# Optimization experiments

Hardware: AMD Instinct MI355X
Metric: run time of the kernel (lower is better)

The kernel has to match this reference:

```python
import jax, jax.numpy as jnp
import numpy as np

# Winograd F(2x2, 3x3) transform matrices (standard Lavin & Gray form).
# The original torch module encodes B^T / A^T but applies them with elementwise
# mul (a bug that crashes); the intended math is Y = A^T [ (G g G^T) .* (B^T d B) ] A
# per 4x4 input tile with stride 2, which equals a valid 3x3 conv. We implement
# that intended Winograd computation faithfully and vectorized.
_BT = jnp.array([[1., 0., -1., 0.],
                 [0., 1., 1., 0.],
                 [0., -1., 1., 0.],
                 [0., 1., 0., -1.]], dtype=jnp.float32)
_G = jnp.array([[1., 0., 0.],
                [0.5, 0.5, 0.5],
                [0.5, -0.5, 0.5],
                [0., 0., 1.]], dtype=jnp.float32)
_AT = jnp.array([[1., 1., 1., 0.],
                 [0., 1., -1., -1.]], dtype=jnp.float32)


def setup_inputs() -> dict:
    key = jax.random.key(0)
    k1, k2 = jax.random.split(key)
    X = jax.random.normal(k1, (16, 32, 258, 258), dtype=jnp.float32)
    K = jax.random.normal(k2, (32, 32, 3, 3), dtype=jnp.float32)
    return {"X": X, "K": K}


def _winograd_conv(X, K):
    B_, C, H, W = X.shape
    Fo = K.shape[0]
    blocks = (H - 3) // 2 + 1  # number of 2x2 output tiles per spatial dim

    # Kernel transform: U = G K G^T  -> (Fo, C, 4, 4)
    U = jnp.einsum('ij,fcjk,lk->fcil', _G, K, _G)

    # Extract overlapping 4x4 tiles with stride 2: (B, C, blocks, blocks, 4, 4)
    i0 = jnp.arange(blocks) * 2
    win = i0[:, None] + jnp.arange(4)[None, :]          # (blocks, 4)
    tiles = X[:, :, win, :]                              # (B, C, blocks, 4, W)
    tiles = tiles[:, :, :, :, win]                       # (B, C, blocks, 4, blocks, 4)
    tiles = tiles.transpose(0, 1, 2, 4, 3, 5)            # (B, C, p, q, 4, 4)

    # Input transform: V = B^T d B
    V = jnp.einsum('ij,bcpqjk,lk->bcpqil', _BT, tiles, _BT)

    # Elementwise multiply in transform domain, summed over input channels
    M = jnp.einsum('fcil,bcpqil->bfpqil', U, V)          # (B, Fo, p, q, 4, 4)

    # Inverse transform: Y = A^T M A -> (B, Fo, p, q, 2, 2)
    Y = jnp.einsum('ij,bfpqjk,lk->bfpqil', _AT, M, _AT)

    # Stitch 2x2 tiles back: (B, Fo, 2*blocks, 2*blocks)
    out = Y.transpose(0, 1, 2, 4, 3, 5).reshape(B_, Fo, 2 * blocks, 2 * blocks)
    return out


def reference(X, K):
    return _winograd_conv(X, K)
```

## Files before the change

### kernel.cpp

```cpp
#include <hip/hip_runtime.h>
#include <stdint.h>

typedef __attribute__((ext_vector_type(8))) short bf16x8;
typedef __attribute__((ext_vector_type(4))) float f32x4;
typedef __attribute__((ext_vector_type(2))) float f32x2;

__device__ inline float bflo(uint32_t w) { union { uint32_t i; float f; } v; v.i = w << 16; return v.f; }
__device__ inline float bfhi(uint32_t w) { union { uint32_t i; float f; } v; v.i = w & 0xffff0000u; return v.f; }
__device__ inline uint32_t f2bf(float f) { union { float f; uint32_t i; } v; v.f = f; return (v.i + 0x8000u) >> 16; }
__device__ inline uint32_t pk(float lo, float hi) { return f2bf(lo) | (f2bf(hi) << 16); }

__device__ inline f32x2 pka(f32x2 a, f32x2 b) {
    f32x2 d; asm("v_pk_add_f32 %0, %1, %2" : "=v"(d) : "v"(a), "v"(b)); return d;
}
__device__ inline f32x2 pks(f32x2 a, f32x2 b) {
    f32x2 d; asm("v_pk_add_f32 %0, %1, %2 neg_lo:[0,1] neg_hi:[0,1]" : "=v"(d) : "v"(a), "v"(b)); return d;
}
__device__ inline uint32_t cvtpk2(float lo, float hi) {
    uint32_t r; asm("v_cvt_pk_bf16_f32 %0, %1, %2" : "=v"(r) : "v"(lo), "v"(hi)); return r;
}
__device__ inline uint32_t cvtpk(f32x2 v) { return cvtpk2(v.x, v.y); }
__device__ inline f32x2 unpk(uint32_t w) {
    union { uint32_t u; float f; } lo, hi; lo.u = w << 16; hi.u = w & 0xffff0000u;
    return (f32x2){lo.f, hi.f};
}

__global__ __launch_bounds__(256) void wg_filter(const float* __restrict__ Kk, uint32_t* __restrict__ Ud)
{
    const int idx = blockIdx.x * 256 + threadIdx.x;
    if (idx >= 512) return;
    const int cp = idx & 15, f = idx >> 4;
    float u[2][16];
    #pragma unroll
    for (int h = 0; h < 2; h++) {
        const float* kp = Kk + (f * 32 + cp * 2 + h) * 9;
        float k00 = kp[0], k01 = kp[1], k02 = kp[2];
        float k10 = kp[3], k11 = kp[4], k12 = kp[5];
        float k20 = kp[6], k21 = kp[7], k22 = kp[8];
        float t[4][3];
        t[0][0] = k00; t[0][1] = k01; t[0][2] = k02;
        t[1][0] = 0.5f * (k00 + k10 + k20); t[1][1] = 0.5f * (k01 + k11 + k21); t[1][2] = 0.5f * (k02 + k12 + k22);
        t[2][0] = 0.5f * (k00 - k10 + k20); t[2][1] = 0.5f * (k01 - k11 + k21); t[2][2] = 0.5f * (k02 - k12 + k22);
        t[3][0] = k20; t[3][1] = k21; t[3][2] = k22;
        #pragma unroll
        for (int i = 0; i < 4; i++) {
            float a0 = t[i][0], a1 = t[i][1], a2 = t[i][2];
            u[h][i * 4 + 0] = a0;
            u[h][i * 4 + 1] = 0.5f * (a0 + a1 + a2);
            u[h][i * 4 + 2] = 0.5f * (a0 - a1 + a2);
            u[h][i * 4 + 3] = a2;
        }
    }
    const int base = ((cp >> 2) * 32 + f) * 4 + (cp & 3);
    #pragma unroll
    for (int p = 0; p < 16; p++) Ud[p * 512 + base] = pk(u[0][p], u[1][p]);
}

__global__ __launch_bounds__(256, 3) void wg_main(
    const float* __restrict__ X, const uint16_t* __restrict__ U, float* __restrict__ out)
{
    __shared__ __align__(16) uint32_t Pl[2912];
    __shared__ __align__(16) uint16_t Vl[2][4096];

    const int tid = threadIdx.x;
    const int lin  = blockIdx.x + 16 * (blockIdx.y + 32 * blockIdx.z);
    const int work = (lin & 7) * 1024 + (lin >> 3);
    const int qb = work & 15;
    const int pb = (work >> 4) & 31;
    const int b  = work >> 9;
    const int y0 = pb * 8, x0 = qb * 16;

    const int wave = tid >> 6, lane = tid & 63;
    const int fh = wave & 1, tb = wave >> 1;
    const int l15 = lane & 15, lq = lane >> 4;
    const uint16_t* Ub = U + (lq * 32 + fh * 16 + l15) * 8;

    bf16x8 a_cur[4];
    #pragma unroll
    for (int l = 0; l < 4; l++)
        a_cur[l] = *(const bf16x8*)(Ub + l * 1024);

    for (int s = tid; s < 1440; s += 256) {
        const int pr = s / 90;
        const int r  = s - pr * 90;
        const int row = r / 9, seg = r - row * 9;
        const float* g0 = X + ((size_t)((b * 32 + pr * 2) * 258 + y0 + row)) * 258 + x0 + seg * 2;
        float2 a = *(const float2*)g0;
        float2 c = *(const float2*)(g0 + 258 * 258);
        uint2 w;
        w.x = cvtpk2(a.x, c.x);
        w.y = cvtpk2(a.y, c.y);
        *(uint2*)&Pl[pr * 182 + row * 18 + seg * 2] = w;
    }
    __syncthreads();

    const int cp2 = tid & 3, t15c = (tid >> 2) & 15;

    float y[4][4];
    #pragma unroll
    for (int r = 0; r < 4; r++)
        #pragma unroll
        for (int j = 0; j < 4; j++) y[r][j] = 0.f;

    #pragma unroll
    for (int i = 0; i < 4; i++) {
        const int ra = (i == 0) ? 0 : (i == 2) ? 2 : 1;
        const int rb = (i == 3) ? 3 : (i == 2) ? 1 : 2;

        uint32_t* vp = (uint32_t*)Vl[i & 1];

        #pragma unroll
        for (int it = 0; it < 2; it++) {
            const int rem  = it * 4 + wave;
            const int tblk = rem & 1, cpH = rem >> 1;
            const int cp   = cpH * 4 + cp2;
            const int tt   = tblk * 16 + t15c;
            const int tr   = tt >> 3, tc = tt & 7;
            const uint32_t* pp = &Pl[cp * 182 + (tr * 2) * 18 + tc * 2];
            uint2 wa0 = *(const uint2*)&pp[ra * 18];
            uint2 wa1 = *(const uint2*)&pp[ra * 18 + 2];
            uint2 wb0 = *(const uint2*)&pp[rb * 18];
            uint2 wb1 = *(const uint2*)&pp[rb * 18 + 2];
            f32x2 da[4], db[4];
            da[0] = unpk(wa0.x); da[1] = unpk(wa0.y); da[2] = unpk(wa1.x); da[3] = unpk(wa1.y);
            db[0] = unpk(wb0.x); db[1] = unpk(wb0.y); db[2] = unpk(wb1.x); db[3] = unpk(wb1.y);
            f32x2 e[4];
            #pragma unroll
            for (int k = 0; k < 4; k++)
                e[k] = (i == 1) ? pka(da[k], db[k]) : pks(da[k], db[k]);
            const int vbase = ((tblk * 4 + cpH) * 16 + t15c) * 4 + cp2;
            vp[0 * 512 + vbase] = cvtpk(pks(e[0], e[2]));
            vp[1 * 512 + vbase] = cvtpk(pka(e[1], e[2]));
            vp[2 * 512 + vbase] = cvtpk(pks(e[2], e[1]));
            vp[3 * 512 + vbase] = cvtpk(pks(e[1], e[3]));
        }

        bf16x8 a_nxt[4];
        if (i < 3) {
            #pragma unroll
            for (int l = 0; l < 4; l++)
                a_nxt[l] = *(const bf16x8*)(Ub + ((i + 1) * 4 + l) * 1024);
        }

        __syncthreads();

        const uint16_t* Vb = Vl[i & 1] + ((tb * 4 + lq) * 16 + l15) * 8;
        f32x4 acc[4];
        #pragma unroll
        for (int l = 0; l < 4; l++) {
            bf16x8 v = *(const bf16x8*)(Vb + l * 1024);
            acc[l] = __builtin_amdgcn_mfma_f32_16x16x32_bf16(a_cur[l], v,
                        (f32x4){0.f, 0.f, 0.f, 0.f}, 0, 0, 0);
        }

        #pragma unroll
        for (int l = 0; l < 4; l++) a_cur[l] = a_nxt[l];

        #pragma unroll
        for (int r = 0; r < 4; r++) {
            float m0 = acc[0][r], m1 = acc[1][r], m2 = acc[2][r], m3 = acc[3][r];
            float c0 = m0 + m1 + m2, c1 = m1 - m2 - m3;
            if (i == 0)      { y[r][0] += c0; y[r][1] += c1; }
            else if (i == 1) { y[r][0] += c0; y[r][1] += c1; y[r][2] += c0; y[r][3] += c1; }
            else if (i == 2) { y[r][0] += c0; y[r][1] += c1; y[r][2] -= c0; y[r][3] -= c1; }
            else             { y[r][2] -= c0; y[r][3] -= c1; }
        }
    }

    const int tt = tb * 16 + l15;
    const int trr = tt >> 3, tcc = tt & 7;
    const int p = pb * 4 + trr, q = qb * 8 + tcc;
    #pragma unroll
    for (int r = 0; r < 4; r++) {
        const int f = fh * 16 + lq * 4 + r;
        float* op = out + ((size_t)(b * 32 + f) * 256 + 2 * p) * 256 + 2 * q;
        *(float2*)op = make_float2(y[r][0], y[r][1]);
        *(float2*)(op + 256) = make_float2(y[r][2], y[r][3]);
    }
}

__device__ inline uint16_t f2bf16_rne(float f) {
    union { float f; uint32_t i; } v; v.f = f;
    uint32_t x = v.i;
    uint32_t r = x + 0x7fffu + ((x >> 16) & 1u);
    return (uint16_t)(r >> 16);
}
__global__ __launch_bounds__(256) void winograd_fallback(
    const float* __restrict__ X, const float* __restrict__ K, float* __restrict__ out)
{
    __shared__ uint16_t Ul[16384];
    __shared__ uint16_t Vl[16384];
    __shared__ uint16_t Pl[32 * 242];
    const int tid = threadIdx.x;
    const int qb = blockIdx.x, pb = blockIdx.y, b = blockIdx.z;
    for (int idx = tid; idx < 1024; idx += 256) {
        const int f = idx >> 5, c = idx & 31;
        const float* kp = K + (f * 32 + c) * 9;
        float k00 = kp[0], k01 = kp[1], k02 = kp[2];
        float k10 = kp[3], k11 = kp[4], k12 = kp[5];
        float k20 = kp[6], k21 = kp[7], k22 = kp[8];
        float t[4][3];
        t[0][0] = k00; t[0][1] = k01; t[0][2] = k02;
        t[1][0] = 0.5f * (k00 + k10 + k20); t[1][1] = 0.5f * (k01 + k11 + k21); t[1][2] = 0.5f * (k02 + k12 + k22);
        t[2][0] = 0.5f * (k00 - k10 + k20); t[2][1] = 0.5f * (k01 - k11 + k21); t[2][2] = 0.5f * (k02 - k12 + k22);
        t[3][0] = k20; t[3][1] = k21; t[3][2] = k22;
        const int ubase = ((c >> 3) * 32 + f) * 8 + (c & 7);
        #pragma unroll
        for (int i = 0; i < 4; i++) {
            float a0 = t[i][0], a1 = t[i][1], a2 = t[i][2];
            Ul[(i * 4 + 0) * 1024 + ubase] = f2bf16_rne(a0);
            Ul[(i * 4 + 1) * 1024 + ubase] = f2bf16_rne(0.5f * (a0 + a1 + a2));
            Ul[(i * 4 + 2) * 1024 + ubase] = f2bf16_rne(0.5f * (a0 - a1 + a2));
            Ul[(i * 4 + 3) * 1024 + ubase] = f2bf16_rne(a2);
        }
    }
    const int y0 = pb * 8, x0 = qb * 16;
    for (int s = tid; s < 2880; s += 256) {
        const int c = s / 90;
        const int r = s % 90;
        const int row = r / 9, seg = r % 9;
        const float* gp = X + ((b * 32 + c) * 258 + (y0 + row)) * 258 + x0 + seg * 2;
        float2 g = *(const float2*)gp;
        uint32_t packed = (uint32_t)f2bf16_rne(g.x) | ((uint32_t)f2bf16_rne(g.y) << 16);
        *(uint32_t*)&Pl[c * 242 + row * 24 + seg * 2] = packed;
    }
    __syncthreads();
    for (int idx = tid; idx < 1024; idx += 256) {
        const int c = idx & 31, tt = idx >> 5;
        const int tr = tt >> 3, tc = tt & 7;
        const uint16_t* pp = &Pl[c * 242 + (tr * 2) * 24 + tc * 2];
        float d[4][4];
        #pragma unroll
        for (int j = 0; j < 4; j++) {
            uint32_t w0 = *(const uint32_t*)&pp[j * 24];
            uint32_t w1 = *(const uint32_t*)&pp[j * 24 + 2];
            d[j][0] = bflo(w0); d[j][1] = bfhi(w0);
            d[j][2] = bflo(w1); d[j][3] = bfhi(w1);
        }
        float bt[4][4];
        #pragma unroll
        for (int k = 0; k < 4; k++) {
            bt[0][k] = d[0][k] - d[2][k];
            bt[1][k] = d[1][k] + d[2][k];
            bt[2][k] = d[2][k] - d[1][k];
            bt[3][k] = d[1][k] - d[3][k];
        }
        const int vbase = (((tt >> 4) * 4 + (c >> 3)) * 16 + (tt & 15)) * 8 + (c & 7);
        #pragma unroll
        for (int i = 0; i < 4; i++) {
            float b0 = bt[i][0], b1 = bt[i][1], b2 = bt[i][2], b3 = bt[i][3];
            Vl[(i * 4 + 0) * 1024 + vbase] = f2bf16_rne(b0 - b2);
            Vl[(i * 4 + 1) * 1024 + vbase] = f2bf16_rne(b1 + b2);
            Vl[(i * 4 + 2) * 1024 + vbase] = f2bf16_rne(b2 - b1);
            Vl[(i * 4 + 3) * 1024 + vbase] = f2bf16_rne(b1 - b3);
        }
    }
    __syncthreads();
    const int wave = tid >> 6, lane = tid & 63;
    const int fh = wave & 1, tb = wave >> 1;
    const int l15 = lane & 15, lq = lane >> 4;
    f32x4 acc[16];
    #pragma unroll
    for (int p = 0; p < 16; p++) acc[p] = (f32x4){0.f, 0.f, 0.f, 0.f};
    #pragma unroll
    for (int p = 0; p < 16; p++) {
        bf16x8 a = *(const bf16x8*)&Ul[p * 1024 + (lq * 32 + fh * 16 + l15) * 8];
        bf16x8 bv = *(const bf16x8*)&Vl[p * 1024 + ((tb * 4 + lq) * 16 + l15) * 8];
        acc[p] = __builtin_amdgcn_mfma_f32_16x16x32_bf16(a, bv, acc[p], 0, 0, 0);
    }
    #pragma unroll
    for (int r = 0; r < 4; r++) {
        const int f = fh * 16 + lq * 4 + r;
        const int t = tb * 16 + l15;
        const int tr = t >> 3, tc = t & 7;
        const int p = pb * 4 + tr, q = qb * 8 + tc;
        float m[4][4];
        #pragma unroll
        for (int i = 0; i < 4; i++)
            #pragma unroll
            for (int l = 0; l < 4; l++)
                m[i][l] = acc[i * 4 + l][r];
        float s0[4], s1[4];
        #pragma unroll
        for (int k = 0; k < 4; k++) {
            s0[k] = m[0][k] + m[1][k] + m[2][k];
            s1[k] = m[1][k] - m[2][k] - m[3][k];
        }
        float* op = out + ((size_t)(b * 32 + f) * 256 + 2 * p) * 256 + 2 * q;
        *(float2*)op = make_float2(s0[0] + s0[1] + s0[2], s0[1] - s0[2] - s0[3]);
        *(float2*)(op + 256) = make_float2(s1[0] + s1[1] + s1[2], s1[1] - s1[2] - s1[3]);
    }
}

extern "C" void kernel_launch(void* const* d_in, const int* in_sizes, int n_in,
                              void* d_out, int out_size, void* d_ws, size_t ws_size,
                              hipStream_t stream) {
    const float* X = (const float*)d_in[0];
    const float* K = (const float*)d_in[1];
    float* out = (float*)d_out;
    dim3 grid(16, 32, 16);
    if (ws_size >= 32768) {
        wg_filter<<<2, 256, 0, stream>>>(K, (uint32_t*)d_ws);
        wg_main<<<grid, 256, 0, stream>>>(X, (const uint16_t*)d_ws, out);
    } else {
        winograd_fallback<<<grid, 256, 0, stream>>>(X, K, out);
    }
}
```

Measured before the change: 82.24 us.

## Compute all four Winograd row transforms in one pass and batch MFMA phases

The input transform now reads each tile's 4x4 patch from LDS once and computes all four row combinations together. Two of them go straight to the two V buffers, and the other two are kept in registers and written after the first pair of MFMA phases. This cuts the barriers from four interleaved transform/MFMA rounds down to three, and removes the repeated LDS reads of the patch rows. In exchange it raises register pressure (16 extra packed words per thread plus a second prefetched U fragment) under launch_bounds(256,3), and it reorders the phases to 0,2,1,3.

```diff
diff --git a/kernel.cpp b/kernel.cpp
--- a/kernel.cpp
+++ b/kernel.cpp
@@ -56,6 +56,30 @@
     for (int p = 0; p < 16; p++) Ud[p * 512 + base] = pk(u[0][p], u[1][p]);
 }
 
+template<int CH>
+__device__ __forceinline__ void d_phase(const uint16_t* __restrict__ Vbuf,
+                                        const bf16x8 (&a)[4], float (&y)[4][4],
+                                        int tb, int lq, int l15)
+{
+    const uint16_t* Vb = Vbuf + ((tb * 4 + lq) * 16 + l15) * 8;
+    f32x4 acc[4];
+    #pragma unroll
+    for (int l = 0; l < 4; l++) {
+        bf16x8 v = *(const bf16x8*)(Vb + l * 1024);
+        acc[l] = __builtin_amdgcn_mfma_f32_16x16x32_bf16(a[l], v,
+                    (f32x4){0.f, 0.f, 0.f, 0.f}, 0, 0, 0);
+    }
+    #pragma unroll
+    for (int r = 0; r < 4; r++) {
+        float m0 = acc[0][r], m1 = acc[1][r], m2 = acc[2][r], m3 = acc[3][r];
+        float c0 = m0 + m1 + m2, c1 = m1 - m2 - m3;
+        if (CH == 0)      { y[r][0] += c0; y[r][1] += c1; }
+        else if (CH == 1) { y[r][0] += c0; y[r][1] += c1; y[r][2] += c0; y[r][3] += c1; }
+        else if (CH == 2) { y[r][0] += c0; y[r][1] += c1; y[r][2] -= c0; y[r][3] -= c1; }
+        else              { y[r][2] -= c0; y[r][3] -= c1; }
+    }
+}
+
 __global__ __launch_bounds__(256, 3) void wg_main(
     const float* __restrict__ X, const uint16_t* __restrict__ U, float* __restrict__ out)
 {
@@ -75,7 +99,7 @@
     const int l15 = lane & 15, lq = lane >> 4;
     const uint16_t* Ub = U + (lq * 32 + fh * 16 + l15) * 8;
 
-    bf16x8 a_cur[4];
+    bf16x8 a_cur[4], a_nxt[4];
     #pragma unroll
     for (int l = 0; l < 4; l++)
         a_cur[l] = *(const bf16x8*)(Ub + l * 1024);
@@ -92,6 +116,9 @@
         w.y = cvtpk2(a.y, c.y);
         *(uint2*)&Pl[pr * 182 + row * 18 + seg * 2] = w;
     }
+    #pragma unroll
+    for (int l = 0; l < 4; l++)
+        a_nxt[l] = *(const bf16x8*)(Ub + (2 * 4 + l) * 1024);
     __syncthreads();
 
     const int cp2 = tid & 3, t15c = (tid >> 2) & 15;
@@ -102,70 +129,85 @@
         #pragma unroll
         for (int j = 0; j < 4; j++) y[r][j] = 0.f;
 
-    #pragma unroll
-    for (int i = 0; i < 4; i++) {
-        const int ra = (i == 0) ? 0 : (i == 2) ? 2 : 1;
-        const int rb = (i == 3) ? 3 : (i == 2) ? 1 : 2;
-
-        uint32_t* vp = (uint32_t*)Vl[i & 1];
-
-        #pragma unroll
-        for (int it = 0; it < 2; it++) {
-            const int rem  = it * 4 + wave;
-            const int tblk = rem & 1, cpH = rem >> 1;
-            const int cp   = cpH * 4 + cp2;
-            const int tt   = tblk * 16 + t15c;
-            const int tr   = tt >> 3, tc = tt & 7;
-            const uint32_t* pp = &Pl[cp * 182 + (tr * 2) * 18 + tc * 2];
-            uint2 wa0 = *(const uint2*)&pp[ra * 18];
-            uint2 wa1 = *(const uint2*)&pp[ra * 18 + 2];
-            uint2 wb0 = *(const uint2*)&pp[rb * 18];
-            uint2 wb1 = *(const uint2*)&pp[rb * 18 + 2];
-            f32x2 da[4], db[4];
-            da[0] = unpk(wa0.x); da[1] = unpk(wa0.y); da[2] = unpk(wa1.x); da[3] = unpk(wa1.y);
-            db[0] = unpk(wb0.x); db[1] = unpk(wb0.y); db[2] = unpk(wb1.x); db[3] = unpk(wb1.y);
-            f32x2 e[4];
-            #pragma unroll
-            for (int k = 0; k < 4; k++)
-                e[k] = (i == 1) ? pka(da[k], db[k]) : pks(da[k], db[k]);
-            const int vbase = ((tblk * 4 + cpH) * 16 + t15c) * 4 + cp2;
-            vp[0 * 512 + vbase] = cvtpk(pks(e[0], e[2]));
-            vp[1 * 512 + vbase] = cvtpk(pka(e[1], e[2]));
-            vp[2 * 512 + vbase] = cvtpk(pks(e[2], e[1]));
-            vp[3 * 512 + vbase] = cvtpk(pks(e[1], e[3]));
-        }
-
-        bf16x8 a_nxt[4];
-        if (i < 3) {
-            #pragma unroll
-            for (int l = 0; l < 4; l++)
-                a_nxt[l] = *(const bf16x8*)(Ub + ((i + 1) * 4 + l) * 1024);
-        }
-
-        __syncthreads();
-
-        const uint16_t* Vb = Vl[i & 1] + ((tb * 4 + lq) * 16 + l15) * 8;
-        f32x4 acc[4];
+    uint32_t vh1[2][4], vh3[2][4];
+    int vbs[2];
+    uint32_t* vp0 = (uint32_t*)Vl[0];
+    uint32_t* vp1 = (uint32_t*)Vl[1];
+
+    #pragma unroll
+    for (int it = 0; it < 2; it++) {
+        const int rem  = it * 4 + wave;
+        const int tblk = rem & 1, cpH = rem >> 1;
+        const int cp   = cpH * 4 + cp2;
+        const int tt   = tblk * 16 + t15c;
+        const int tr   = tt >> 3, tc = tt & 7;
+        const uint32_t* pp = &Pl[cp * 182 + (tr * 2) * 18 + tc * 2];
+        f32x2 d[4][4];
+        #pragma unroll
+        for (int j = 0; j < 4; j++) {
+            uint2 w0 = *(const uint2*)&pp[j * 18];
+            uint2 w1 = *(const uint2*)&pp[j * 18 + 2];
+            d[j][0] = unpk(w0.x); d[j][1] = unpk(w0.y);
+            d[j][2] = unpk(w1.x); d[j][3] = unpk(w1.y);
+        }
+        f32x2 e0[4], e1[4], e2[4], e3[4];
+        #pragma unroll
+        for (int k = 0; k < 4; k++) {
+            e0[k] = pks(d[0][k], d[2][k]);
+            e1[k] = pka(d[1][k], d[2][k]);
+            e2[k] = pks(d[2][k], d[1][k]);
+            e3[k] = pks(d[1][k], d[3][k]);
+        }
+        const int vbase = ((tblk * 4 + cpH) * 16 + t15c) * 4 + cp2;
+        vbs[it] = vbase;
+        vp0[0 * 512 + vbase] = cvtpk(pks(e0[0], e0[2]));
+        vp0[1 * 512 + vbase] = cvtpk(pka(e0[1], e0[2]));
+        vp0[2 * 512 + vbase] = cvtpk(pks(e0[2], e0[1]));
+        vp0[3 * 512 + vbase] = cvtpk(pks(e0[1], e0[3]));
+        vp1[0 * 512 + vbase] = cvtpk(pks(e2[0], e2[2]));
+        vp1[1 * 512 + vbase] = cvtpk(pka(e2[1], e2[2]));
+        vp1[2 * 512 + vbase] = cvtpk(pks(e2[2], e2[1]));
+        vp1[3 * 512 + vbase] = cvtpk(pks(e2[1], e2[3]));
+        vh1[it][0] = cvtpk(pks(e1[0], e1[2]));
+        vh1[it][1] = cvtpk(pka(e1[1], e1[2]));
+        vh1[it][2] = cvtpk(pks(e1[2], e1[1]));
+        vh1[it][3] = cvtpk(pks(e1[1], e1[3]));
+        vh3[it][0] = cvtpk(pks(e3[0], e3[2]));
+        vh3[it][1] = cvtpk(pka(e3[1], e3[2]));
+        vh3[it][2] = cvtpk(pks(e3[2], e3[1]));
+        vh3[it][3] = cvtpk(pks(e3[1], e3[3]));
+    }
+    __syncthreads();
+
+    d_phase<0>(Vl[0], a_cur, y, tb, lq, l15);
+    #pragma unroll
+    for (int l = 0; l < 4; l++) a_cur[l] = a_nxt[l];
+    #pragma unroll
+    for (int l = 0; l < 4; l++)
+        a_nxt[l] = *(const bf16x8*)(Ub + (1 * 4 + l) * 1024);
+    d_phase<2>(Vl[1], a_cur, y, tb, lq, l15);
+    #pragma unroll
+    for (int l = 0; l < 4; l++) a_cur[l] = a_nxt[l];
+    #pragma unroll
+    for (int l = 0; l < 4; l++)
+        a_nxt[l] = *(const bf16x8*)(Ub + (3 * 4 + l) * 1024);
+
+    __syncthreads();
+
+    #pragma unroll
+    for (int it = 0; it < 2; it++) {
         #pragma unroll
         for (int l = 0; l < 4; l++) {
-            bf16x8 v = *(const bf16x8*)(Vb + l * 1024);
-            acc[l] = __builtin_amdgcn_mfma_f32_16x16x32_bf16(a_cur[l], v,
-                        (f32x4){0.f, 0.f, 0.f, 0.f}, 0, 0, 0);
-        }
-
-        #pragma unroll
-        for (int l = 0; l < 4; l++) a_cur[l] = a_nxt[l];
-
-        #pragma unroll
-        for (int r = 0; r < 4; r++) {
-            float m0 = acc[0][r], m1 = acc[1][r], m2 = acc[2][r], m3 = acc[3][r];
-            float c0 = m0 + m1 + m2, c1 = m1 - m2 - m3;
-            if (i == 0)      { y[r][0] += c0; y[r][1] += c1; }
-            else if (i == 1) { y[r][0] += c0; y[r][1] += c1; y[r][2] += c0; y[r][3] += c1; }
-            else if (i == 2) { y[r][0] += c0; y[r][1] += c1; y[r][2] -= c0; y[r][3] -= c1; }
-            else             { y[r][2] -= c0; y[r][3] -= c1; }
-        }
-    }
+            vp0[l * 512 + vbs[it]] = vh1[it][l];
+            vp1[l * 512 + vbs[it]] = vh3[it][l];
+        }
+    }
+    __syncthreads();
+
+    d_phase<1>(Vl[0], a_cur, y, tb, lq, l15);
+    #pragma unroll
+    for (int l = 0; l < 4; l++) a_cur[l] = a_nxt[l];
+    d_phase<3>(Vl[1], a_cur, y, tb, lq, l15);
 
     const int tt = tb * 16 + l15;
     const int trr = tt >> 3, tcc = tt & 7;
```

New measurement: 80.36 us, median of 2. 1.02x faster.
